# Kernel optimization log

Measured on AMD Instinct MI355X. Metric: run time of the kernel, lower is better.

## Reference

```python
import jax, jax.numpy as jnp
import numpy as np

DIST_THRESH = 0.1
W_DIST = 0.05
W_CHAMFER = 0.05
W_SEP = 0.0005


def setup_inputs() -> dict:
    key = jax.random.key(0)
    k1, k2, k3, k4 = jax.random.split(key, 4)
    B, N, K = 4, 200000, 64
    return {
        "landmarks_C": jax.random.uniform(k1, (B, N, 3), jnp.float32),          # predicted point coords
        "landmarks_F": jax.random.normal(k2, (B, N, 4), jnp.float32) * 0.05,    # [dist, dx, dy, dz]
        "targets_C": jax.random.uniform(k3, (B, K, 3), jnp.float32),            # GT landmark coords
        "targets_F": jax.random.randint(k4, (B, K), 0, 8),                      # GT landmark class labels
        "classes": jnp.arange(6),                                               # classes to supervise
    }


def reference(landmarks_C, landmarks_F, targets_C, targets_F, classes):
    def per_batch(C_i, F_i, tC, tF):
        # class mask over GT landmarks (replaces boolean indexing in torch)
        mask_k = jnp.any(tF[None, :] == classes[:, None], axis=0)          # [K]
        n_valid = mask_k.sum()
        dists_i = F_i[:, 0]                                                # predicted distance, [N]
        coords_i = C_i + F_i[:, 1:]                                        # refined coords, [N,3]
        # pairwise dists GT landmarks -> raw point coords, invalid classes pushed to +inf
        pd = jnp.linalg.norm(C_i[None, :, :] - tC[:, None, :], axis=-1)    # [K,N]
        pd = jnp.where(mask_k[:, None], pd, jnp.inf)
        min_d = pd.min(axis=0)                                             # [N]
        pm = min_d < DIST_THRESH                                           # points near some GT landmark
        # smooth-L1 (beta=1, sum) on predicted distance; clip(inf)=2*thresh reproduces empty-target fallback
        tgt = jnp.clip(min_d, 0.0, 2.0 * DIST_THRESH)
        diff = dists_i - tgt
        ad = jnp.abs(diff)
        dist_loss = jnp.where(ad < 1.0, 0.5 * diff * diff, ad - 0.5).sum()
        # pairwise dists GT landmarks -> refined coords
        ld = jnp.linalg.norm(coords_i[None, :, :] - tC[:, None, :], axis=-1)  # [K,N]
        ld_m = jnp.where(mask_k[:, None], ld, jnp.inf)
        p2g = jnp.where(pm, ld_m.min(axis=0), 0.0)                         # pred->gt, masked points only
        g2p = jnp.where(mask_k, ld_m.min(axis=1), 0.0)                     # gt->pred, valid GT only
        chamfer = (p2g * p2g).sum() + (g2p * g2p).sum()
        # separation: ratio of dists to 2 nearest (valid) GT landmarks, per masked point
        _, idx = jax.lax.top_k(-pd.T, 2)                                   # [N,2] indices of 2 smallest
        d01 = jnp.take_along_axis(ld.T, idx, axis=1)                       # [N,2]
        sep = jnp.where(pm, d01[:, 0] / d01[:, 1], 0.0).sum()
        sep = jnp.where(n_valid >= 2, sep, 0.0)
        return W_DIST * dist_loss + W_CHAMFER * chamfer + W_SEP * sep

    losses = jax.vmap(per_batch)(landmarks_C, landmarks_F, targets_C, targets_F)
    return losses.mean()
```

## Files before the change

### kernel.cpp

```cpp
#include <hip/hip_runtime.h>


constexpr int KT = 64;
constexpr int P  = 4;
constexpr int NREP = 16;
constexpr float DIST_THRESH = 0.1f;
constexpr float W_DIST    = 0.05f;
constexpr float W_CHAMFER = 0.05f;
constexpr float W_SEP     = 0.0005f;
constexpr float PT_SENT = -1e18f;
constexpr float TG_SENT = -1e18f;
constexpr float BIGF  = 3.0e38f;
constexpr float WBIAS = 16.0f;

typedef float f2 __attribute__((ext_vector_type(2)));

__device__ __forceinline__ unsigned umin_(unsigned a, unsigned b) { return a < b ? a : b; }
__device__ __forceinline__ unsigned umax_(unsigned a, unsigned b) { return a > b ? a : b; }

__device__ __forceinline__ f2 pk_fma(f2 a, f2 b, f2 c) {
#if __has_builtin(__builtin_elementwise_fma)
    return __builtin_elementwise_fma(a, b, c);
#else
    f2 r; r.x = fmaf(a.x, b.x, c.x); r.y = fmaf(a.y, b.y, c.y); return r;
#endif
}

__global__ __launch_bounds__(128, 4)
void landmark_main(const float* __restrict__ C, const float* __restrict__ F,
                   const float* __restrict__ tC, const int* __restrict__ tF,
                   const int* __restrict__ classes, int n_classes, int N,
                   unsigned int* __restrict__ g2p_rep, float* __restrict__ sums_rep)
{
    __shared__ float4   tgtFull[KT];
    __shared__ unsigned g2pLDS[KT];
    __shared__ uint4    mK1[64], mK2[64];
    __shared__ float4   mLM[64];

    const int tid   = threadIdx.x;
    const int lane  = tid & 63;
    const int h     = tid >> 6;
    const int l31   = lane & 31;
    const int hi5   = lane >> 5;
    const int blk   = blockIdx.x;
    const int b     = blk & 3;
    const int pair  = blk >> 2;
    const int rep   = pair & (NREP - 1);

    if (tid < KT) {
        int f = tF[b * KT + tid];
        bool valid = false;
        for (int c = 0; c < n_classes; ++c) valid = valid || (f == classes[c]);
        float x = TG_SENT, y = TG_SENT, z = TG_SENT;
        if (valid) {
            x = tC[(b * KT + tid) * 3 + 0];
            y = tC[(b * KT + tid) * 3 + 1];
            z = tC[(b * KT + tid) * 3 + 2];
        }
        tgtFull[tid] = make_float4(-2.f * x, -2.f * y, -2.f * z,
                                   x * x + y * y + z * z + WBIAS);
        g2pLDS[tid] = 0x7F7FFFFFu;
    }
    __syncthreads();

    const float*  Cb = C + (size_t)b * N * 3;
    const float4* Fb = (const float4*)(F + (size_t)b * N * 4);
    const int base0 = pair * 512;
    const int base1 = base0 + 256;

    float4 rf[P]; float rX[P], rY[P], rZ[P];
    f2 pcx[P], pcy[P], pcz[P];
    float ppm[P], ccm[P], f0[P];
    unsigned k1[P], k2[P];
    float lmin[P];
    float dist_acc = 0.f, p2g_acc = 0.f, sep_acc = 0.f;

    auto issue_loads = [&](int baseN) {
        #pragma unroll
        for (int p = 0; p < P; ++p) {
            int n = baseN + p * 64 + lane;
            int ni = (n < N) ? n : 0;
            rf[p] = Fb[ni];
            rX[p] = Cb[3 * ni + 0];
            rY[p] = Cb[3 * ni + 1];
            rZ[p] = Cb[3 * ni + 2];
        }
    };
    auto process = [&](int baseN) {
        #pragma unroll
        for (int p = 0; p < P; ++p) {
            int n = baseN + p * 64 + lane;
            bool v = (n < N);
            float4 f4 = rf[p];
            float X = rX[p], Y = rY[p], Z = rZ[p];
            f0[p] = v ? f4.x : 2.0f * DIST_THRESH;
            if (!v) { X = PT_SENT; Y = PT_SENT; Z = PT_SENT; f4.y = f4.z = f4.w = 0.f; }
            float cxv = X + f4.y, cyv = Y + f4.z, czv = Z + f4.w;
            pcx[p] = (f2){X, cxv};
            pcy[p] = (f2){Y, cyv};
            pcz[p] = (f2){Z, czv};
            ppm[p] = fmaf(Z, Z, fmaf(Y, Y, X * X)) - WBIAS;
            ccm[p] = fmaf(czv, czv, fmaf(cyv, cyv, cxv * cxv)) - WBIAS;
        }
    };

    const unsigned tkb = (unsigned)((l31 ^ (hi5 << 4)) | (h << 5));

    auto do_chunk = [&]() {
        #pragma unroll
        for (int p = 0; p < P; ++p) { k1[p] = 0xFFFFFFFFu; k2[p] = 0xFFFFFFFFu; lmin[p] = BIGF; }

        #pragma unroll 8
        for (int i = 0; i < 32; ++i) {
            const unsigned tk = tkb ^ (unsigned)i;
            const float4 T = tgtFull[tk];
            const f2 Tx = {T.x, T.x}, Ty = {T.y, T.y}, Tz = {T.z, T.z}, Tw = {T.w, T.w};
            float av[P];
            #pragma unroll
            for (int p = 0; p < P; ++p) {
                f2 w2 = pk_fma(pcx[p], Tx, pk_fma(pcy[p], Ty, pk_fma(pcz[p], Tz, Tw)));
                unsigned key = (__float_as_uint(w2.x) & 0xFFFFFFC0u) | tk;
                unsigned hi = umax_(k1[p], key);
                k1[p] = umin_(k1[p], key);
                k2[p] = umin_(k2[p], hi);
                lmin[p] = fminf(lmin[p], w2.y);
                av[p] = w2.y + ccm[p];
            }
            float dl = fmaxf(fminf(fminf(av[0], av[1]), fminf(av[2], av[3])), 0.f);
            atomicMin(&g2pLDS[tk], __float_as_uint(dl));
        }

        if (h == 0) {
            mK1[lane] = make_uint4(k1[0], k1[1], k1[2], k1[3]);
            mK2[lane] = make_uint4(k2[0], k2[1], k2[2], k2[3]);
            mLM[lane] = make_float4(lmin[0], lmin[1], lmin[2], lmin[3]);
        }
        __syncthreads();

        if (h == 1) {
            uint4 A1 = mK1[lane], A2 = mK2[lane];
            float4 AL = mLM[lane];
            const unsigned a1v[P] = {A1.x, A1.y, A1.z, A1.w};
            const unsigned a2v[P] = {A2.x, A2.y, A2.z, A2.w};
            const float    alv[P] = {AL.x, AL.y, AL.z, AL.w};
            #pragma unroll
            for (int p = 0; p < P; ++p) {
                unsigned m1 = umin_(a1v[p], k1[p]);
                unsigned m2 = umin_(umax_(a1v[p], k1[p]), umin_(a2v[p], k2[p]));
                float lm = fminf(alv[p], lmin[p]);
                float keyf1 = __uint_as_float(m1 & 0xFFFFFFC0u);
                float mind = sqrtf(fmaxf(keyf1 + ppm[p], 0.f));
                bool pm = mind < DIST_THRESH;
                float tgtv = fminf(mind, 2.0f * DIST_THRESH);
                float diff = f0[p] - tgtv;
                float ad = fabsf(diff);
                dist_acc += (ad < 1.0f) ? 0.5f * diff * diff : (ad - 0.5f);
                if (pm) {
                    p2g_acc += fmaxf(lm + ccm[p], 0.f);
                    int i1 = (int)(m1 & 63u), i2 = (int)(m2 & 63u);
                    float4 T1 = tgtFull[i1], T2 = tgtFull[i2];
                    float cxv = pcx[p].y, cyv = pcy[p].y, czv = pcz[p].y;
                    float l1sq = fmaf(cxv, T1.x, fmaf(cyv, T1.y, fmaf(czv, T1.z, T1.w))) + ccm[p];
                    float l2sq = fmaf(cxv, T2.x, fmaf(cyv, T2.y, fmaf(czv, T2.z, T2.w))) + ccm[p];
                    sep_acc += sqrtf(fmaxf(l1sq, 0.f) / fmaxf(l2sq, 1e-30f));
                }
            }
        }
        __syncthreads();
    };

    issue_loads(base0);
    process(base0);
    issue_loads(base1);
    do_chunk();
    process(base1);
    do_chunk();

    if (h == 0) {
        atomicMax(&g2p_rep[rep * 256 + b * 64 + lane], ~g2pLDS[lane]);
    } else {
        float v0 = dist_acc, v1 = p2g_acc, v2 = sep_acc;
        #pragma unroll
        for (int o = 32; o > 0; o >>= 1) {
            v0 += __shfl_down(v0, o, 64);
            v1 += __shfl_down(v1, o, 64);
            v2 += __shfl_down(v2, o, 64);
        }
        if (lane == 0) {
            float* sb = sums_rep + rep * 16 + b;
            atomicAdd(sb + 0, v0);
            atomicAdd(sb + 4, v1);
            atomicAdd(sb + 8, v2);
        }
    }
}

__global__ void landmark_finalize(const int* __restrict__ tF, const int* __restrict__ classes,
                                  int n_classes, const unsigned int* __restrict__ g2p_rep,
                                  const float* __restrict__ sums_rep, float* __restrict__ out)
{
    __shared__ float lossb[4];
    const int tid = threadIdx.x;
    const int b = tid >> 6, k = tid & 63;

    int f = tF[b * KT + k];
    bool valid = false;
    for (int c = 0; c < n_classes; ++c) valid = valid || (f == classes[c]);

    unsigned enc = 0;
    for (int r = 0; r < NREP; ++r) enc = umax_(enc, g2p_rep[r * 256 + b * 64 + k]);
    float g  = valid ? __uint_as_float(~enc) : 0.f;
    float nv = valid ? 1.f : 0.f;

    #pragma unroll
    for (int o = 32; o > 0; o >>= 1) {
        g  += __shfl_down(g, o, 64);
        nv += __shfl_down(nv, o, 64);
    }
    if (k == 0) {
        float sd = 0.f, sp = 0.f, ss = 0.f;
        for (int r = 0; r < NREP; ++r) {
            sd += sums_rep[r * 16 + 0 + b];
            sp += sums_rep[r * 16 + 4 + b];
            ss += sums_rep[r * 16 + 8 + b];
        }
        float sep = (nv >= 2.f) ? ss : 0.f;
        lossb[b] = W_DIST * sd + W_CHAMFER * (sp + g) + W_SEP * sep;
    }
    __syncthreads();
    if (tid == 0)
        out[0] = (lossb[0] + lossb[1] + lossb[2] + lossb[3]) * 0.25f;
}

extern "C" void kernel_launch(void* const* d_in, const int* in_sizes, int n_in,
                              void* d_out, int out_size, void* d_ws, size_t ws_size,
                              hipStream_t stream)
{
    const float* C       = (const float*)d_in[0];
    const float* F       = (const float*)d_in[1];
    const float* tC      = (const float*)d_in[2];
    const int*   tF      = (const int*)d_in[3];
    const int*   classes = (const int*)d_in[4];
    const int n_classes = in_sizes[4];
    const int B = 4;
    const int N = in_sizes[0] / (3 * B);

    unsigned int* g2p_rep  = (unsigned int*)d_ws;
    float*        sums_rep = (float*)((char*)d_ws + NREP * 256 * 4);

    hipMemsetAsync(d_ws, 0, NREP * 256 * 4 + NREP * 16 * 4, stream);

    const int pairs = (N + 511) / 512;
    landmark_main<<<pairs * 4, 128, 0, stream>>>(C, F, tC, tF, classes, n_classes,
                                                 N, g2p_rep, sums_rep);
    landmark_finalize<<<1, 256, 0, stream>>>(tF, classes, n_classes, g2p_rep,
                                             sums_rep, (float*)d_out);
}
```

Before: 101.6 us.

## Process one 256-point chunk per block and prefetch target tiles from LDS

Each block now handles a single 256-point chunk instead of two, which doubles the grid and removes the second do_chunk pass and its pair of block barriers. Point loads are issued before the target-setup code so global latency overlaps the class-mask work, and target float4s are double-buffered from LDS in groups of four. The cost is more blocks, so more per-block setup (target table build, LDS init) and twice as many global atomics into g2p_rep and sums_rep.

```diff
diff --git a/kernel.cpp b/kernel.cpp
--- a/kernel.cpp
+++ b/kernel.cpp
@@ -44,76 +44,79 @@
     const int hi5   = lane >> 5;
     const int blk   = blockIdx.x;
     const int b     = blk & 3;
-    const int pair  = blk >> 2;
-    const int rep   = pair & (NREP - 1);
+    const int chunk = blk >> 2;
+    const int rep   = chunk & (NREP - 1);
+
+    const float*  Cb = C + (size_t)b * N * 3;
+    const float4* Fb = (const float4*)(F + (size_t)b * N * 4);
+    const int base = chunk * (64 * P);
+
+    float4 rf[P]; float rX[P], rY[P], rZ[P];
+    #pragma unroll
+    for (int p = 0; p < P; ++p) {
+        int n = base + p * 64 + lane;
+        int ni = (n < N) ? n : 0;
+        rf[p] = Fb[ni];
+        rX[p] = Cb[3 * ni + 0];
+        rY[p] = Cb[3 * ni + 1];
+        rZ[p] = Cb[3 * ni + 2];
+    }
 
     if (tid < KT) {
         int f = tF[b * KT + tid];
+        float x = tC[(b * KT + tid) * 3 + 0];
+        float y = tC[(b * KT + tid) * 3 + 1];
+        float z = tC[(b * KT + tid) * 3 + 2];
         bool valid = false;
         for (int c = 0; c < n_classes; ++c) valid = valid || (f == classes[c]);
-        float x = TG_SENT, y = TG_SENT, z = TG_SENT;
-        if (valid) {
-            x = tC[(b * KT + tid) * 3 + 0];
-            y = tC[(b * KT + tid) * 3 + 1];
-            z = tC[(b * KT + tid) * 3 + 2];
-        }
+        if (!valid) { x = TG_SENT; y = TG_SENT; z = TG_SENT; }
         tgtFull[tid] = make_float4(-2.f * x, -2.f * y, -2.f * z,
                                    x * x + y * y + z * z + WBIAS);
         g2pLDS[tid] = 0x7F7FFFFFu;
     }
     __syncthreads();
 
-    const float*  Cb = C + (size_t)b * N * 3;
-    const float4* Fb = (const float4*)(F + (size_t)b * N * 4);
-    const int base0 = pair * 512;
-    const int base1 = base0 + 256;
-
-    float4 rf[P]; float rX[P], rY[P], rZ[P];
     f2 pcx[P], pcy[P], pcz[P];
     float ppm[P], ccm[P], f0[P];
+    #pragma unroll
+    for (int p = 0; p < P; ++p) {
+        int n = base + p * 64 + lane;
+        bool v = (n < N);
+        float4 f4 = rf[p];
+        float X = rX[p], Y = rY[p], Z = rZ[p];
+        f0[p] = v ? f4.x : 2.0f * DIST_THRESH;
+        if (!v) { X = PT_SENT; Y = PT_SENT; Z = PT_SENT; f4.y = f4.z = f4.w = 0.f; }
+        float cxv = X + f4.y, cyv = Y + f4.z, czv = Z + f4.w;
+        pcx[p] = (f2){X, cxv};
+        pcy[p] = (f2){Y, cyv};
+        pcz[p] = (f2){Z, czv};
+        ppm[p] = fmaf(Z, Z, fmaf(Y, Y, X * X)) - WBIAS;
+        ccm[p] = fmaf(czv, czv, fmaf(cyv, cyv, cxv * cxv)) - WBIAS;
+    }
+
     unsigned k1[P], k2[P];
     float lmin[P];
-    float dist_acc = 0.f, p2g_acc = 0.f, sep_acc = 0.f;
-
-    auto issue_loads = [&](int baseN) {
+    #pragma unroll
+    for (int p = 0; p < P; ++p) { k1[p] = 0xFFFFFFFFu; k2[p] = 0xFFFFFFFFu; lmin[p] = BIGF; }
+
+    const unsigned tkb = (unsigned)((l31 ^ (hi5 << 4)) | (h << 5));
+
+    float4 Tb[2][4];
+    #pragma unroll
+    for (int j = 0; j < 4; ++j) Tb[0][j] = tgtFull[tkb ^ (unsigned)j];
+
+    #pragma unroll
+    for (int g = 0; g < 8; ++g) {
+        const int cur = g & 1, nxt = cur ^ 1;
+        if (g < 7) {
+            #pragma unroll
+            for (int j = 0; j < 4; ++j)
+                Tb[nxt][j] = tgtFull[tkb ^ (unsigned)((g + 1) * 4 + j)];
+        }
         #pragma unroll
-        for (int p = 0; p < P; ++p) {
-            int n = baseN + p * 64 + lane;
-            int ni = (n < N) ? n : 0;
-            rf[p] = Fb[ni];
-            rX[p] = Cb[3 * ni + 0];
-            rY[p] = Cb[3 * ni + 1];
-            rZ[p] = Cb[3 * ni + 2];
-        }
-    };
-    auto process = [&](int baseN) {
-        #pragma unroll
-        for (int p = 0; p < P; ++p) {
-            int n = baseN + p * 64 + lane;
-            bool v = (n < N);
-            float4 f4 = rf[p];
-            float X = rX[p], Y = rY[p], Z = rZ[p];
-            f0[p] = v ? f4.x : 2.0f * DIST_THRESH;
-            if (!v) { X = PT_SENT; Y = PT_SENT; Z = PT_SENT; f4.y = f4.z = f4.w = 0.f; }
-            float cxv = X + f4.y, cyv = Y + f4.z, czv = Z + f4.w;
-            pcx[p] = (f2){X, cxv};
-            pcy[p] = (f2){Y, cyv};
-            pcz[p] = (f2){Z, czv};
-            ppm[p] = fmaf(Z, Z, fmaf(Y, Y, X * X)) - WBIAS;
-            ccm[p] = fmaf(czv, czv, fmaf(cyv, cyv, cxv * cxv)) - WBIAS;
-        }
-    };
-
-    const unsigned tkb = (unsigned)((l31 ^ (hi5 << 4)) | (h << 5));
-
-    auto do_chunk = [&]() {
-        #pragma unroll
-        for (int p = 0; p < P; ++p) { k1[p] = 0xFFFFFFFFu; k2[p] = 0xFFFFFFFFu; lmin[p] = BIGF; }
-
-        #pragma unroll 8
-        for (int i = 0; i < 32; ++i) {
-            const unsigned tk = tkb ^ (unsigned)i;
-            const float4 T = tgtFull[tk];
+        for (int j = 0; j < 4; ++j) {
+            const unsigned tk = tkb ^ (unsigned)(g * 4 + j);
+            const float4 T = Tb[cur][j];
             const f2 Tx = {T.x, T.x}, Ty = {T.y, T.y}, Tz = {T.z, T.z}, Tw = {T.w, T.w};
             float av[P];
             #pragma unroll
@@ -129,56 +132,48 @@
             float dl = fmaxf(fminf(fminf(av[0], av[1]), fminf(av[2], av[3])), 0.f);
             atomicMin(&g2pLDS[tk], __float_as_uint(dl));
         }
-
-        if (h == 0) {
-            mK1[lane] = make_uint4(k1[0], k1[1], k1[2], k1[3]);
-            mK2[lane] = make_uint4(k2[0], k2[1], k2[2], k2[3]);
-            mLM[lane] = make_float4(lmin[0], lmin[1], lmin[2], lmin[3]);
-        }
-        __syncthreads();
-
-        if (h == 1) {
-            uint4 A1 = mK1[lane], A2 = mK2[lane];
-            float4 AL = mLM[lane];
-            const unsigned a1v[P] = {A1.x, A1.y, A1.z, A1.w};
-            const unsigned a2v[P] = {A2.x, A2.y, A2.z, A2.w};
-            const float    alv[P] = {AL.x, AL.y, AL.z, AL.w};
-            #pragma unroll
-            for (int p = 0; p < P; ++p) {
-                unsigned m1 = umin_(a1v[p], k1[p]);
-                unsigned m2 = umin_(umax_(a1v[p], k1[p]), umin_(a2v[p], k2[p]));
-                float lm = fminf(alv[p], lmin[p]);
-                float keyf1 = __uint_as_float(m1 & 0xFFFFFFC0u);
-                float mind = sqrtf(fmaxf(keyf1 + ppm[p], 0.f));
-                bool pm = mind < DIST_THRESH;
-                float tgtv = fminf(mind, 2.0f * DIST_THRESH);
-                float diff = f0[p] - tgtv;
-                float ad = fabsf(diff);
-                dist_acc += (ad < 1.0f) ? 0.5f * diff * diff : (ad - 0.5f);
-                if (pm) {
-                    p2g_acc += fmaxf(lm + ccm[p], 0.f);
-                    int i1 = (int)(m1 & 63u), i2 = (int)(m2 & 63u);
-                    float4 T1 = tgtFull[i1], T2 = tgtFull[i2];
-                    float cxv = pcx[p].y, cyv = pcy[p].y, czv = pcz[p].y;
-                    float l1sq = fmaf(cxv, T1.x, fmaf(cyv, T1.y, fmaf(czv, T1.z, T1.w))) + ccm[p];
-                    float l2sq = fmaf(cxv, T2.x, fmaf(cyv, T2.y, fmaf(czv, T2.z, T2.w))) + ccm[p];
-                    sep_acc += sqrtf(fmaxf(l1sq, 0.f) / fmaxf(l2sq, 1e-30f));
-                }
-            }
-        }
-        __syncthreads();
-    };
-
-    issue_loads(base0);
-    process(base0);
-    issue_loads(base1);
-    do_chunk();
-    process(base1);
-    do_chunk();
+    }
+
+    if (h == 0) {
+        mK1[lane] = make_uint4(k1[0], k1[1], k1[2], k1[3]);
+        mK2[lane] = make_uint4(k2[0], k2[1], k2[2], k2[3]);
+        mLM[lane] = make_float4(lmin[0], lmin[1], lmin[2], lmin[3]);
+    }
+    __syncthreads();
 
     if (h == 0) {
         atomicMax(&g2p_rep[rep * 256 + b * 64 + lane], ~g2pLDS[lane]);
     } else {
+        uint4 A1 = mK1[lane], A2 = mK2[lane];
+        float4 AL = mLM[lane];
+        const unsigned a1v[P] = {A1.x, A1.y, A1.z, A1.w};
+        const unsigned a2v[P] = {A2.x, A2.y, A2.z, A2.w};
+        const float    alv[P] = {AL.x, AL.y, AL.z, AL.w};
+
+        float dist_acc = 0.f, p2g_acc = 0.f, sep_acc = 0.f;
+        #pragma unroll
+        for (int p = 0; p < P; ++p) {
+            unsigned m1 = umin_(a1v[p], k1[p]);
+            unsigned m2 = umin_(umax_(a1v[p], k1[p]), umin_(a2v[p], k2[p]));
+            float lm = fminf(alv[p], lmin[p]);
+            float keyf1 = __uint_as_float(m1 & 0xFFFFFFC0u);
+            float mind = sqrtf(fmaxf(keyf1 + ppm[p], 0.f));
+            bool pm = mind < DIST_THRESH;
+            float tgtv = fminf(mind, 2.0f * DIST_THRESH);
+            float diff = f0[p] - tgtv;
+            float ad = fabsf(diff);
+            dist_acc += (ad < 1.0f) ? 0.5f * diff * diff : (ad - 0.5f);
+            if (pm) {
+                p2g_acc += fmaxf(lm + ccm[p], 0.f);
+                int i1 = (int)(m1 & 63u), i2 = (int)(m2 & 63u);
+                float4 T1 = tgtFull[i1], T2 = tgtFull[i2];
+                float cxv = pcx[p].y, cyv = pcy[p].y, czv = pcz[p].y;
+                float l1sq = fmaf(cxv, T1.x, fmaf(cyv, T1.y, fmaf(czv, T1.z, T1.w))) + ccm[p];
+                float l2sq = fmaf(cxv, T2.x, fmaf(cyv, T2.y, fmaf(czv, T2.z, T2.w))) + ccm[p];
+                sep_acc += sqrtf(fmaxf(l1sq, 0.f) / fmaxf(l2sq, 1e-30f));
+            }
+        }
+
         float v0 = dist_acc, v1 = p2g_acc, v2 = sep_acc;
         #pragma unroll
         for (int o = 32; o > 0; o >>= 1) {
@@ -250,9 +245,9 @@
 
     hipMemsetAsync(d_ws, 0, NREP * 256 * 4 + NREP * 16 * 4, stream);
 
-    const int pairs = (N + 511) / 512;
-    landmark_main<<<pairs * 4, 128, 0, stream>>>(C, F, tC, tF, classes, n_classes,
-                                                 N, g2p_rep, sums_rep);
+    const int cpb = (N + 64 * P - 1) / (64 * P);
+    landmark_main<<<cpb * 4, 128, 0, stream>>>(C, F, tC, tF, classes, n_classes,
+                                               N, g2p_rep, sums_rep);
     landmark_finalize<<<1, 256, 0, stream>>>(tF, classes, n_classes, g2p_rep,
                                              sums_rep, (float*)d_out);
 }
```

New measurement: 97.21 us, median of 2. 1.05x faster.
